# Kernel tuning notes

Hardware: AMD Instinct MI355X
Metric: run time of the kernel (lower is better)

The kernel has to match this reference:

```python
import jax, jax.numpy as jnp
import numpy as np


def _per_sample_ce(logits, targets):
    # -log_softmax(logits)[i, targets[i]]  -> shape [N]
    logp = jax.nn.log_softmax(logits, axis=-1)
    return -jnp.take_along_axis(logp, targets[:, None], axis=-1)[:, 0]


def setup_inputs() -> dict:
    key = jax.random.key(0)
    k1, k2, k3 = jax.random.split(key, 3)
    N, C = 65536, 1000
    y_1 = jax.random.normal(k1, (N, C), dtype=jnp.float32)
    y_2 = jax.random.normal(k2, (N, C), dtype=jnp.float32)
    targets = jax.random.randint(k3, (N,), 0, C, dtype=jnp.int64)
    num_keep = 45875  # int(0.7 * N), static for jit
    return {"y_1": y_1, "y_2": y_2, "targets": targets, "num_keep": num_keep}


def reference(y_1, y_2, targets, num_keep):
    loss_1 = _per_sample_ce(y_1, targets)          # [N]
    loss_2 = _per_sample_ce(y_2, targets)          # [N]
    # small-loss selection: indices of the num_keep smallest per-sample losses
    ind_1_update = jnp.argsort(loss_1)[:num_keep]  # selected by net 1
    ind_2_update = jnp.argsort(loss_2)[:num_keep]  # selected by net 2
    # cross-update: each net trains on the peer's selected samples
    loss_1_update = _per_sample_ce(y_1[ind_2_update], targets[ind_2_update])
    loss_2_update = _per_sample_ce(y_2[ind_1_update], targets[ind_1_update])
    # size_average=True -> means
    return (loss_1_update.mean(), loss_2_update.mean(),
            loss_1.mean(), loss_2.mean())
```

## Files before the change

kernel.cpp:

```cpp
#include <hip/hip_runtime.h>
#include <math.h>

#define MAXT 4096

struct SelState {
  unsigned prefix;
  unsigned rank;
  unsigned tieCount;
  int cutoff;
};

__device__ __forceinline__ unsigned keyOf(float f) {
  unsigned b = __float_as_uint(f);
  return b ^ ((b & 0x80000000u) ? 0xFFFFFFFFu : 0x80000000u);
}

__device__ __forceinline__ float waveMax(float v) {
#pragma unroll
  for (int o = 32; o >= 1; o >>= 1) v = fmaxf(v, __shfl_xor(v, o));
  return v;
}
__device__ __forceinline__ float waveSum(float v) {
#pragma unroll
  for (int o = 32; o >= 1; o >>= 1) v += __shfl_xor(v, o);
  return v;
}

__global__ __launch_bounds__(256) void init_kernel(unsigned* __restrict__ h1,
                                                   unsigned* __restrict__ h2,
                                                   SelState* st1, SelState* st2,
                                                   const int* __restrict__ numKeep) {
  int t = threadIdx.x;
  for (int j = t; j < 2048; j += 256) { h1[j] = 0u; h2[j] = 0u; }
  if (t == 0) {
    unsigned k = (unsigned)(*numKeep);
    st1->prefix = 0u; st1->rank = k; st1->tieCount = 0u; st1->cutoff = -1;
    st2->prefix = 0u; st2->rank = k; st2->tieCount = 0u; st2->cutoff = -1;
  }
}

__global__ __launch_bounds__(256) void ce_kernel(
    const float* __restrict__ y1, const float* __restrict__ y2,
    const int* __restrict__ tgt,
    float* __restrict__ l1, float* __restrict__ l2, int N) {
  const float L2E = 1.4426950408889634f;
  const float LN2 = 0.6931471805599453f;
  int wid = threadIdx.x >> 6, lane = threadIdx.x & 63;
  int row = blockIdx.x * 4 + wid;
  if (row >= N) return;
  int t = tgt[row];
  int vecIdx = t >> 2;
  int grp = vecIdx >> 6;
  int srcLane = vecIdx & 63;
  int comp = t & 3;
#pragma unroll
  for (int which = 0; which < 2; ++which) {
    const float* y = which ? y2 : y1;
    const float4* rp = (const float4*)(y + (size_t)row * 1000);
    float4 a = rp[lane];
    float4 b = rp[lane + 64];
    float4 c = rp[lane + 128];
    float4 d = make_float4(-INFINITY, -INFINITY, -INFINITY, -INFINITY);
    if (lane + 192 < 250) d = rp[lane + 192];
    float4 sel = (grp == 0) ? a : (grp == 1) ? b : (grp == 2) ? c : d;
    float cand = (comp == 0) ? sel.x : (comp == 1) ? sel.y
               : (comp == 2) ? sel.z : sel.w;
    float xt = __shfl(cand, srcLane);
    float m = fmaxf(fmaxf(fmaxf(a.x, a.y), fmaxf(a.z, a.w)),
                    fmaxf(fmaxf(b.x, b.y), fmaxf(b.z, b.w)));
    m = fmaxf(m, fmaxf(fmaxf(c.x, c.y), fmaxf(c.z, c.w)));
    m = fmaxf(m, fmaxf(fmaxf(d.x, d.y), fmaxf(d.z, d.w)));
    m = waveMax(m);
    float s = exp2f((a.x - m) * L2E) + exp2f((a.y - m) * L2E) +
              exp2f((a.z - m) * L2E) + exp2f((a.w - m) * L2E) +
              exp2f((b.x - m) * L2E) + exp2f((b.y - m) * L2E) +
              exp2f((b.z - m) * L2E) + exp2f((b.w - m) * L2E) +
              exp2f((c.x - m) * L2E) + exp2f((c.y - m) * L2E) +
              exp2f((c.z - m) * L2E) + exp2f((c.w - m) * L2E) +
              exp2f((d.x - m) * L2E) + exp2f((d.y - m) * L2E) +
              exp2f((d.z - m) * L2E) + exp2f((d.w - m) * L2E);
    s = waveSum(s);
    if (lane == 0) {
      float loss = log2f(s) * LN2 + m - xt;
      (which ? l2 : l1)[row] = loss;
    }
  }
}

__global__ __launch_bounds__(256) void histA_kernel(
    const float* __restrict__ l1, const float* __restrict__ l2,
    unsigned* __restrict__ h1, unsigned* __restrict__ h2, int N) {
  __shared__ unsigned lh[2][2048];
  int t = threadIdx.x;
  for (int j = t; j < 2048; j += 256) { lh[0][j] = 0u; lh[1][j] = 0u; }
  __syncthreads();
  for (int i = blockIdx.x * blockDim.x + t; i < N;
       i += gridDim.x * blockDim.x) {
    atomicAdd(&lh[0][keyOf(l1[i]) >> 21], 1u);
    atomicAdd(&lh[1][keyOf(l2[i]) >> 21], 1u);
  }
  __syncthreads();
  for (int j = t; j < 2048; j += 256) {
    unsigned v0 = lh[0][j], v1 = lh[1][j];
    if (v0) atomicAdd(&h1[j], v0);
    if (v1) atomicAdd(&h2[j], v1);
  }
}

__global__ __launch_bounds__(256) void hist_kernel(
    const float* __restrict__ l1, const float* __restrict__ l2,
    unsigned* __restrict__ h1, unsigned* __restrict__ h2,
    const SelState* __restrict__ st1, const SelState* __restrict__ st2,
    int N, int shift, unsigned binMask, unsigned mmask) {
  unsigned p1 = st1->prefix, p2 = st2->prefix;
  for (int i = blockIdx.x * blockDim.x + threadIdx.x; i < N;
       i += gridDim.x * blockDim.x) {
    unsigned k1 = keyOf(l1[i]);
    if ((k1 & mmask) == p1) atomicAdd(&h1[(k1 >> shift) & binMask], 1u);
    unsigned k2 = keyOf(l2[i]);
    if ((k2 & mmask) == p2) atomicAdd(&h2[(k2 >> shift) & binMask], 1u);
  }
}

__global__ __launch_bounds__(256) void scan_kernel(
    unsigned* __restrict__ h1, unsigned* __restrict__ h2,
    SelState* __restrict__ st1, SelState* __restrict__ st2,
    int shift, int nbits) {
  unsigned* h = blockIdx.x ? h2 : h1;
  SelState* st = blockIdx.x ? st2 : st1;
  int t = threadIdx.x;
  int bins = 1 << nbits;
  int per = bins >> 8;
  unsigned r = st->rank;
  unsigned pfx = st->prefix;
  unsigned local[8];
  unsigned s = 0;
  for (int j = 0; j < per; ++j) { local[j] = h[t * per + j]; s += local[j]; }
  __shared__ unsigned sc[256];
  sc[t] = s;
  __syncthreads();
  for (int off = 1; off < 256; off <<= 1) {
    unsigned v = (t >= off) ? sc[t - off] : 0u;
    __syncthreads();
    sc[t] += v;
    __syncthreads();
  }
  unsigned incl = sc[t];
  unsigned excl = incl - s;
  if (excl < r && r <= incl) {
    unsigned cum = excl;
    for (int j = 0; j < per; ++j) {
      if (cum + local[j] >= r) {
        st->prefix = pfx | ((unsigned)(t * per + j) << shift);
        st->rank = r - cum;
        break;
      }
      cum += local[j];
    }
  }
  __syncthreads();
  for (int j = 0; j < per; ++j) h[t * per + j] = 0u;
}

__global__ __launch_bounds__(256) void tiecollect_kernel(
    const float* __restrict__ l1, const float* __restrict__ l2,
    SelState* st1, SelState* st2, int* __restrict__ t1, int* __restrict__ t2,
    int N) {
  unsigned K1 = st1->prefix, K2 = st2->prefix;
  for (int i = blockIdx.x * blockDim.x + threadIdx.x; i < N;
       i += gridDim.x * blockDim.x) {
    if (keyOf(l1[i]) == K1) {
      unsigned p = atomicAdd(&st1->tieCount, 1u);
      if (p < MAXT) t1[p] = i;
    }
    if (keyOf(l2[i]) == K2) {
      unsigned p = atomicAdd(&st2->tieCount, 1u);
      if (p < MAXT) t2[p] = i;
    }
  }
}

__global__ __launch_bounds__(256) void tierank_kernel(SelState* st1,
                                                      SelState* st2,
                                                      const int* __restrict__ t1,
                                                      const int* __restrict__ t2) {
  SelState* st = blockIdx.x ? st2 : st1;
  const int* ti = blockIdx.x ? t2 : t1;
  int T = min((int)st->tieCount, MAXT);
  int need = (int)st->rank;
  if (need >= T) {
    if (threadIdx.x == 0) st->cutoff = 0x7FFFFFFF;
    return;
  }
  for (int j = threadIdx.x; j < T; j += 256) {
    int idx = ti[j];
    int rk = 0;
    for (int m = 0; m < T; ++m) rk += (ti[m] < idx) ? 1 : 0;
    if (rk == need - 1) st->cutoff = idx;
  }
}

__global__ __launch_bounds__(256) void partial_kernel(
    const float* __restrict__ l1, const float* __restrict__ l2,
    const SelState* __restrict__ st1, const SelState* __restrict__ st2,
    float* __restrict__ partials, int N) {
  unsigned K1 = st1->prefix, K2 = st2->prefix;
  int c1 = st1->cutoff, c2 = st2->cutoff;
  float s0 = 0.f, s1 = 0.f, s2 = 0.f, s3 = 0.f;
  for (int i = blockIdx.x * blockDim.x + threadIdx.x; i < N;
       i += gridDim.x * blockDim.x) {
    float f1 = l1[i], f2 = l2[i];
    unsigned k1 = keyOf(f1), k2 = keyOf(f2);
    bool sel1 = (k1 < K1) || (k1 == K1 && i <= c1);
    bool sel2 = (k2 < K2) || (k2 == K2 && i <= c2);
    if (sel2) s0 += f1;
    if (sel1) s1 += f2;
    s2 += f1;
    s3 += f2;
  }
  s0 = waveSum(s0); s1 = waveSum(s1); s2 = waveSum(s2); s3 = waveSum(s3);
  __shared__ float red[4][4];
  int wid = threadIdx.x >> 6, lane = threadIdx.x & 63;
  if (lane == 0) {
    red[wid][0] = s0; red[wid][1] = s1; red[wid][2] = s2; red[wid][3] = s3;
  }
  __syncthreads();
  if (threadIdx.x == 0) {
    for (int q = 0; q < 4; ++q)
      partials[blockIdx.x * 4 + q] =
          red[0][q] + red[1][q] + red[2][q] + red[3][q];
  }
}

__global__ __launch_bounds__(256) void final_kernel(
    const float* __restrict__ partials, const int* __restrict__ numKeep,
    float* __restrict__ out, int N, int nBlocks) {
  float s0 = 0.f, s1 = 0.f, s2 = 0.f, s3 = 0.f;
  for (int j = threadIdx.x; j < nBlocks; j += 256) {
    s0 += partials[j * 4 + 0];
    s1 += partials[j * 4 + 1];
    s2 += partials[j * 4 + 2];
    s3 += partials[j * 4 + 3];
  }
  s0 = waveSum(s0); s1 = waveSum(s1); s2 = waveSum(s2); s3 = waveSum(s3);
  __shared__ float red[4][4];
  int wid = threadIdx.x >> 6, lane = threadIdx.x & 63;
  if (lane == 0) {
    red[wid][0] = s0; red[wid][1] = s1; red[wid][2] = s2; red[wid][3] = s3;
  }
  __syncthreads();
  if (threadIdx.x == 0) {
    float a0 = red[0][0] + red[1][0] + red[2][0] + red[3][0];
    float a1 = red[0][1] + red[1][1] + red[2][1] + red[3][1];
    float a2 = red[0][2] + red[1][2] + red[2][2] + red[3][2];
    float a3 = red[0][3] + red[1][3] + red[2][3] + red[3][3];
    float k = (float)(*numKeep);
    out[0] = a0 / k;
    out[1] = a1 / k;
    out[2] = a2 / (float)N;
    out[3] = a3 / (float)N;
  }
}

extern "C" void kernel_launch(void* const* d_in, const int* in_sizes, int n_in,
                              void* d_out, int out_size, void* d_ws,
                              size_t ws_size, hipStream_t stream) {
  const float* y1 = (const float*)d_in[0];
  const float* y2 = (const float*)d_in[1];
  const int* tgt = (const int*)d_in[2];
  const int* numKeep = (const int*)d_in[3];
  int N = in_sizes[2];
  float* out = (float*)d_out;

  float* l1 = (float*)d_ws;
  float* l2 = l1 + N;
  unsigned* h1 = (unsigned*)(l2 + N);
  unsigned* h2 = h1 + 2048;
  SelState* st1 = (SelState*)(h2 + 2048);
  SelState* st2 = st1 + 1;
  int* t1 = (int*)(st2 + 1);
  int* t2 = t1 + MAXT;
  float* partials = (float*)(t2 + MAXT);

  init_kernel<<<1, 256, 0, stream>>>(h1, h2, st1, st2, numKeep);
  ce_kernel<<<(N + 3) / 4, 256, 0, stream>>>(y1, y2, tgt, l1, l2, N);
  histA_kernel<<<256, 256, 0, stream>>>(l1, l2, h1, h2, N);
  scan_kernel<<<2, 256, 0, stream>>>(h1, h2, st1, st2, 21, 11);
  hist_kernel<<<256, 256, 0, stream>>>(l1, l2, h1, h2, st1, st2, N, 10, 2047u,
                                       0xFFE00000u);
  scan_kernel<<<2, 256, 0, stream>>>(h1, h2, st1, st2, 10, 11);
  hist_kernel<<<256, 256, 0, stream>>>(l1, l2, h1, h2, st1, st2, N, 0, 1023u,
                                       0xFFFFFC00u);
  scan_kernel<<<2, 256, 0, stream>>>(h1, h2, st1, st2, 0, 10);
  tiecollect_kernel<<<256, 256, 0, stream>>>(l1, l2, st1, st2, t1, t2, N);
  tierank_kernel<<<2, 256, 0, stream>>>(st1, st2, t1, t2);
  partial_kernel<<<256, 256, 0, stream>>>(l1, l2, st1, st2, partials, N);
  final_kernel<<<1, 256, 0, stream>>>(partials, numKeep, out, N, 256);
}
```

Measured before the change: 137.0 us.

## Fold radix-select scans into histogram kernels and merge tie collection into partial sums

Drops the separate single-block scan kernels by having every block of each histogram pass recompute the prefix scan of the earlier histograms itself, with separate histogram buffers per level. Tie collection moves into the partial-sum pass, which records tied indices and values, and the final kernel ranks the ties and adds the needed tie values. This cuts the launch sequence from twelve kernels to six, along with the serial dependency gaps between them, but every block now repeats up to six scans with many barriers, and the tie buffer is capped at 2048 entries.

```diff
diff --git a/kernel.cpp b/kernel.cpp
--- a/kernel.cpp
+++ b/kernel.cpp
@@ -1,14 +1,7 @@
 #include <hip/hip_runtime.h>
 #include <math.h>
 
-#define MAXT 4096
-
-struct SelState {
-  unsigned prefix;
-  unsigned rank;
-  unsigned tieCount;
-  int cutoff;
-};
+#define MAXT 2048
 
 __device__ __forceinline__ unsigned keyOf(float f) {
   unsigned b = __float_as_uint(f);
@@ -26,17 +19,41 @@
   return v;
 }
 
-__global__ __launch_bounds__(256) void init_kernel(unsigned* __restrict__ h1,
-                                                   unsigned* __restrict__ h2,
-                                                   SelState* st1, SelState* st2,
-                                                   const int* __restrict__ numKeep) {
+__device__ __forceinline__ void selectStep(const unsigned* __restrict__ h,
+                                           int per, unsigned rank,
+                                           unsigned* sc, unsigned* res) {
   int t = threadIdx.x;
-  for (int j = t; j < 2048; j += 256) { h1[j] = 0u; h2[j] = 0u; }
-  if (t == 0) {
-    unsigned k = (unsigned)(*numKeep);
-    st1->prefix = 0u; st1->rank = k; st1->tieCount = 0u; st1->cutoff = -1;
-    st2->prefix = 0u; st2->rank = k; st2->tieCount = 0u; st2->cutoff = -1;
-  }
+  unsigned local[8];
+  unsigned s = 0;
+  for (int j = 0; j < per; ++j) { local[j] = h[t * per + j]; s += local[j]; }
+  sc[t] = s;
+  __syncthreads();
+  for (int off = 1; off < 256; off <<= 1) {
+    unsigned v = (t >= off) ? sc[t - off] : 0u;
+    __syncthreads();
+    sc[t] += v;
+    __syncthreads();
+  }
+  unsigned incl = sc[t], excl = incl - s;
+  if (excl < rank && rank <= incl) {
+    unsigned cum = excl;
+    for (int j = 0; j < per; ++j) {
+      if (cum + local[j] >= rank) {
+        res[0] = (unsigned)(t * per + j);
+        res[1] = rank - cum;
+        break;
+      }
+      cum += local[j];
+    }
+  }
+  __syncthreads();
+}
+
+__global__ __launch_bounds__(256) void init_kernel(unsigned* __restrict__ hbase,
+                                                   unsigned* __restrict__ tc) {
+  int t = threadIdx.x;
+  for (int j = t; j < 2 * (2048 + 2048 + 1024); j += 256) hbase[j] = 0u;
+  if (t < 2) tc[t] = 0u;
 }
 
 __global__ __launch_bounds__(256) void ce_kernel(
@@ -89,7 +106,7 @@
 
 __global__ __launch_bounds__(256) void histA_kernel(
     const float* __restrict__ l1, const float* __restrict__ l2,
-    unsigned* __restrict__ h1, unsigned* __restrict__ h2, int N) {
+    unsigned* __restrict__ hA1, unsigned* __restrict__ hA2, int N) {
   __shared__ unsigned lh[2][2048];
   int t = threadIdx.x;
   for (int j = t; j < 2048; j += 256) { lh[0][j] = 0u; lh[1][j] = 0u; }
@@ -102,119 +119,93 @@
   __syncthreads();
   for (int j = t; j < 2048; j += 256) {
     unsigned v0 = lh[0][j], v1 = lh[1][j];
-    if (v0) atomicAdd(&h1[j], v0);
-    if (v1) atomicAdd(&h2[j], v1);
-  }
-}
-
-__global__ __launch_bounds__(256) void hist_kernel(
+    if (v0) atomicAdd(&hA1[j], v0);
+    if (v1) atomicAdd(&hA2[j], v1);
+  }
+}
+
+__global__ __launch_bounds__(256) void histB_kernel(
     const float* __restrict__ l1, const float* __restrict__ l2,
-    unsigned* __restrict__ h1, unsigned* __restrict__ h2,
-    const SelState* __restrict__ st1, const SelState* __restrict__ st2,
-    int N, int shift, unsigned binMask, unsigned mmask) {
-  unsigned p1 = st1->prefix, p2 = st2->prefix;
+    const unsigned* __restrict__ hA1, const unsigned* __restrict__ hA2,
+    unsigned* __restrict__ hB1, unsigned* __restrict__ hB2,
+    const int* __restrict__ numKeep, int N) {
+  __shared__ unsigned sc[256];
+  __shared__ unsigned resA1[2], resA2[2];
+  unsigned k0 = (unsigned)(*numKeep);
+  selectStep(hA1, 8, k0, sc, resA1);
+  selectStep(hA2, 8, k0, sc, resA2);
+  unsigned a1 = resA1[0], a2 = resA2[0];
   for (int i = blockIdx.x * blockDim.x + threadIdx.x; i < N;
        i += gridDim.x * blockDim.x) {
     unsigned k1 = keyOf(l1[i]);
-    if ((k1 & mmask) == p1) atomicAdd(&h1[(k1 >> shift) & binMask], 1u);
+    if ((k1 >> 21) == a1) atomicAdd(&hB1[(k1 >> 10) & 2047u], 1u);
     unsigned k2 = keyOf(l2[i]);
-    if ((k2 & mmask) == p2) atomicAdd(&h2[(k2 >> shift) & binMask], 1u);
-  }
-}
-
-__global__ __launch_bounds__(256) void scan_kernel(
-    unsigned* __restrict__ h1, unsigned* __restrict__ h2,
-    SelState* __restrict__ st1, SelState* __restrict__ st2,
-    int shift, int nbits) {
-  unsigned* h = blockIdx.x ? h2 : h1;
-  SelState* st = blockIdx.x ? st2 : st1;
-  int t = threadIdx.x;
-  int bins = 1 << nbits;
-  int per = bins >> 8;
-  unsigned r = st->rank;
-  unsigned pfx = st->prefix;
-  unsigned local[8];
-  unsigned s = 0;
-  for (int j = 0; j < per; ++j) { local[j] = h[t * per + j]; s += local[j]; }
+    if ((k2 >> 21) == a2) atomicAdd(&hB2[(k2 >> 10) & 2047u], 1u);
+  }
+}
+
+__global__ __launch_bounds__(256) void histC_kernel(
+    const float* __restrict__ l1, const float* __restrict__ l2,
+    const unsigned* __restrict__ hA1, const unsigned* __restrict__ hA2,
+    const unsigned* __restrict__ hB1, const unsigned* __restrict__ hB2,
+    unsigned* __restrict__ hC1, unsigned* __restrict__ hC2,
+    const int* __restrict__ numKeep, int N) {
   __shared__ unsigned sc[256];
-  sc[t] = s;
-  __syncthreads();
-  for (int off = 1; off < 256; off <<= 1) {
-    unsigned v = (t >= off) ? sc[t - off] : 0u;
-    __syncthreads();
-    sc[t] += v;
-    __syncthreads();
-  }
-  unsigned incl = sc[t];
-  unsigned excl = incl - s;
-  if (excl < r && r <= incl) {
-    unsigned cum = excl;
-    for (int j = 0; j < per; ++j) {
-      if (cum + local[j] >= r) {
-        st->prefix = pfx | ((unsigned)(t * per + j) << shift);
-        st->rank = r - cum;
-        break;
-      }
-      cum += local[j];
-    }
-  }
-  __syncthreads();
-  for (int j = 0; j < per; ++j) h[t * per + j] = 0u;
-}
-
-__global__ __launch_bounds__(256) void tiecollect_kernel(
-    const float* __restrict__ l1, const float* __restrict__ l2,
-    SelState* st1, SelState* st2, int* __restrict__ t1, int* __restrict__ t2,
-    int N) {
-  unsigned K1 = st1->prefix, K2 = st2->prefix;
+  __shared__ unsigned rA1[2], rA2[2], rB1[2], rB2[2];
+  unsigned k0 = (unsigned)(*numKeep);
+  selectStep(hA1, 8, k0, sc, rA1);
+  selectStep(hA2, 8, k0, sc, rA2);
+  selectStep(hB1, 8, rA1[1], sc, rB1);
+  selectStep(hB2, 8, rA2[1], sc, rB2);
+  unsigned p1 = (rA1[0] << 21) | (rB1[0] << 10);
+  unsigned p2 = (rA2[0] << 21) | (rB2[0] << 10);
   for (int i = blockIdx.x * blockDim.x + threadIdx.x; i < N;
        i += gridDim.x * blockDim.x) {
-    if (keyOf(l1[i]) == K1) {
-      unsigned p = atomicAdd(&st1->tieCount, 1u);
-      if (p < MAXT) t1[p] = i;
-    }
-    if (keyOf(l2[i]) == K2) {
-      unsigned p = atomicAdd(&st2->tieCount, 1u);
-      if (p < MAXT) t2[p] = i;
-    }
-  }
-}
-
-__global__ __launch_bounds__(256) void tierank_kernel(SelState* st1,
-                                                      SelState* st2,
-                                                      const int* __restrict__ t1,
-                                                      const int* __restrict__ t2) {
-  SelState* st = blockIdx.x ? st2 : st1;
-  const int* ti = blockIdx.x ? t2 : t1;
-  int T = min((int)st->tieCount, MAXT);
-  int need = (int)st->rank;
-  if (need >= T) {
-    if (threadIdx.x == 0) st->cutoff = 0x7FFFFFFF;
-    return;
-  }
-  for (int j = threadIdx.x; j < T; j += 256) {
-    int idx = ti[j];
-    int rk = 0;
-    for (int m = 0; m < T; ++m) rk += (ti[m] < idx) ? 1 : 0;
-    if (rk == need - 1) st->cutoff = idx;
+    unsigned k1 = keyOf(l1[i]);
+    if ((k1 & 0xFFFFFC00u) == p1) atomicAdd(&hC1[k1 & 1023u], 1u);
+    unsigned k2 = keyOf(l2[i]);
+    if ((k2 & 0xFFFFFC00u) == p2) atomicAdd(&hC2[k2 & 1023u], 1u);
   }
 }
 
 __global__ __launch_bounds__(256) void partial_kernel(
     const float* __restrict__ l1, const float* __restrict__ l2,
-    const SelState* __restrict__ st1, const SelState* __restrict__ st2,
+    const unsigned* __restrict__ hA1, const unsigned* __restrict__ hA2,
+    const unsigned* __restrict__ hB1, const unsigned* __restrict__ hB2,
+    const unsigned* __restrict__ hC1, const unsigned* __restrict__ hC2,
+    const int* __restrict__ numKeep, unsigned* __restrict__ needs,
+    unsigned* __restrict__ tc, int* __restrict__ tIdx1, float* __restrict__ tVal1,
+    int* __restrict__ tIdx2, float* __restrict__ tVal2,
     float* __restrict__ partials, int N) {
-  unsigned K1 = st1->prefix, K2 = st2->prefix;
-  int c1 = st1->cutoff, c2 = st2->cutoff;
+  __shared__ unsigned sc[256];
+  __shared__ unsigned rA1[2], rA2[2], rB1[2], rB2[2], rC1[2], rC2[2];
+  unsigned k0 = (unsigned)(*numKeep);
+  selectStep(hA1, 8, k0, sc, rA1);
+  selectStep(hA2, 8, k0, sc, rA2);
+  selectStep(hB1, 8, rA1[1], sc, rB1);
+  selectStep(hB2, 8, rA2[1], sc, rB2);
+  selectStep(hC1, 4, rB1[1], sc, rC1);
+  selectStep(hC2, 4, rB2[1], sc, rC2);
+  unsigned K1 = (rA1[0] << 21) | (rB1[0] << 10) | rC1[0];
+  unsigned K2 = (rA2[0] << 21) | (rB2[0] << 10) | rC2[0];
+  if (threadIdx.x == 0) { needs[0] = rC1[1]; needs[1] = rC2[1]; }
   float s0 = 0.f, s1 = 0.f, s2 = 0.f, s3 = 0.f;
   for (int i = blockIdx.x * blockDim.x + threadIdx.x; i < N;
        i += gridDim.x * blockDim.x) {
     float f1 = l1[i], f2 = l2[i];
     unsigned k1 = keyOf(f1), k2 = keyOf(f2);
-    bool sel1 = (k1 < K1) || (k1 == K1 && i <= c1);
-    bool sel2 = (k2 < K2) || (k2 == K2 && i <= c2);
-    if (sel2) s0 += f1;
-    if (sel1) s1 += f2;
+    if (k2 < K2) {
+      s0 += f1;
+    } else if (k2 == K2) {
+      unsigned p = atomicAdd(&tc[1], 1u);
+      if (p < MAXT) { tIdx2[p] = i; tVal2[p] = f1; }
+    }
+    if (k1 < K1) {
+      s1 += f2;
+    } else if (k1 == K1) {
+      unsigned p = atomicAdd(&tc[0], 1u);
+      if (p < MAXT) { tIdx1[p] = i; tVal1[p] = f2; }
+    }
     s2 += f1;
     s3 += f2;
   }
@@ -234,24 +225,49 @@
 
 __global__ __launch_bounds__(256) void final_kernel(
     const float* __restrict__ partials, const int* __restrict__ numKeep,
+    const unsigned* __restrict__ needs, const unsigned* __restrict__ tc,
+    const int* __restrict__ tIdx1, const float* __restrict__ tVal1,
+    const int* __restrict__ tIdx2, const float* __restrict__ tVal2,
     float* __restrict__ out, int N, int nBlocks) {
+  __shared__ float slots[MAXT];
+  __shared__ float red[4][4];
+  __shared__ float tieSum[2];
+  int t = threadIdx.x;
   float s0 = 0.f, s1 = 0.f, s2 = 0.f, s3 = 0.f;
-  for (int j = threadIdx.x; j < nBlocks; j += 256) {
+  for (int j = t; j < nBlocks; j += 256) {
     s0 += partials[j * 4 + 0];
     s1 += partials[j * 4 + 1];
     s2 += partials[j * 4 + 2];
     s3 += partials[j * 4 + 3];
   }
   s0 = waveSum(s0); s1 = waveSum(s1); s2 = waveSum(s2); s3 = waveSum(s3);
-  __shared__ float red[4][4];
-  int wid = threadIdx.x >> 6, lane = threadIdx.x & 63;
+  int wid = t >> 6, lane = t & 63;
   if (lane == 0) {
     red[wid][0] = s0; red[wid][1] = s1; red[wid][2] = s2; red[wid][3] = s3;
   }
-  __syncthreads();
-  if (threadIdx.x == 0) {
-    float a0 = red[0][0] + red[1][0] + red[2][0] + red[3][0];
-    float a1 = red[0][1] + red[1][1] + red[2][1] + red[3][1];
+  for (int a = 0; a < 2; ++a) {
+    const int* ti = a ? tIdx2 : tIdx1;
+    const float* tv = a ? tVal2 : tVal1;
+    int T = min((int)tc[a], MAXT);
+    int need = min((int)needs[a], T);
+    __syncthreads();
+    for (int j = t; j < T; j += 256) {
+      int idx = ti[j];
+      int rk = 0;
+      for (int m = 0; m < T; ++m) rk += (ti[m] < idx) ? 1 : 0;
+      if (rk < need) slots[rk] = tv[j];
+    }
+    __syncthreads();
+    if (t == 0) {
+      float s = 0.f;
+      for (int j = 0; j < need; ++j) s += slots[j];
+      tieSum[a] = s;
+    }
+  }
+  __syncthreads();
+  if (t == 0) {
+    float a0 = red[0][0] + red[1][0] + red[2][0] + red[3][0] + tieSum[1];
+    float a1 = red[0][1] + red[1][1] + red[2][1] + red[3][1] + tieSum[0];
     float a2 = red[0][2] + red[1][2] + red[2][2] + red[3][2];
     float a3 = red[0][3] + red[1][3] + red[2][3] + red[3][3];
     float k = (float)(*numKeep);
@@ -274,26 +290,29 @@
 
   float* l1 = (float*)d_ws;
   float* l2 = l1 + N;
-  unsigned* h1 = (unsigned*)(l2 + N);
-  unsigned* h2 = h1 + 2048;
-  SelState* st1 = (SelState*)(h2 + 2048);
-  SelState* st2 = st1 + 1;
-  int* t1 = (int*)(st2 + 1);
-  int* t2 = t1 + MAXT;
-  float* partials = (float*)(t2 + MAXT);
-
-  init_kernel<<<1, 256, 0, stream>>>(h1, h2, st1, st2, numKeep);
+  unsigned* hA1 = (unsigned*)(l2 + N);
+  unsigned* hA2 = hA1 + 2048;
+  unsigned* hB1 = hA2 + 2048;
+  unsigned* hB2 = hB1 + 2048;
+  unsigned* hC1 = hB2 + 2048;
+  unsigned* hC2 = hC1 + 1024;
+  unsigned* tc = hC2 + 1024;
+  unsigned* needs = tc + 2;
+  int* tIdx1 = (int*)(needs + 2);
+  float* tVal1 = (float*)(tIdx1 + MAXT);
+  int* tIdx2 = (int*)(tVal1 + MAXT);
+  float* tVal2 = (float*)(tIdx2 + MAXT);
+  float* partials = (float*)(tVal2 + MAXT);
+
+  init_kernel<<<1, 256, 0, stream>>>(hA1, tc);
   ce_kernel<<<(N + 3) / 4, 256, 0, stream>>>(y1, y2, tgt, l1, l2, N);
-  histA_kernel<<<256, 256, 0, stream>>>(l1, l2, h1, h2, N);
-  scan_kernel<<<2, 256, 0, stream>>>(h1, h2, st1, st2, 21, 11);
-  hist_kernel<<<256, 256, 0, stream>>>(l1, l2, h1, h2, st1, st2, N, 10, 2047u,
-                                       0xFFE00000u);
-  scan_kernel<<<2, 256, 0, stream>>>(h1, h2, st1, st2, 10, 11);
-  hist_kernel<<<256, 256, 0, stream>>>(l1, l2, h1, h2, st1, st2, N, 0, 1023u,
-                                       0xFFFFFC00u);
-  scan_kernel<<<2, 256, 0, stream>>>(h1, h2, st1, st2, 0, 10);
-  tiecollect_kernel<<<256, 256, 0, stream>>>(l1, l2, st1, st2, t1, t2, N);
-  tierank_kernel<<<2, 256, 0, stream>>>(st1, st2, t1, t2);
-  partial_kernel<<<256, 256, 0, stream>>>(l1, l2, st1, st2, partials, N);
-  final_kernel<<<1, 256, 0, stream>>>(partials, numKeep, out, N, 256);
-}
+  histA_kernel<<<256, 256, 0, stream>>>(l1, l2, hA1, hA2, N);
+  histB_kernel<<<256, 256, 0, stream>>>(l1, l2, hA1, hA2, hB1, hB2, numKeep, N);
+  histC_kernel<<<256, 256, 0, stream>>>(l1, l2, hA1, hA2, hB1, hB2, hC1, hC2,
+                                        numKeep, N);
+  partial_kernel<<<256, 256, 0, stream>>>(l1, l2, hA1, hA2, hB1, hB2, hC1, hC2,
+                                          numKeep, needs, tc, tIdx1, tVal1,
+                                          tIdx2, tVal2, partials, N);
+  final_kernel<<<1, 256, 0, stream>>>(partials, numKeep, needs, tc, tIdx1,
+                                      tVal1, tIdx2, tVal2, out, N, 256);
+}
```

New measurement: 138.1 us. No clear change (+0.8%).
